# Kernel optimization log

Hardware: AMD Instinct MI355X
Metric: run time of the kernel (lower is better)

## Reference

```python
import jax, jax.numpy as jnp
import numpy as np

# Screen constants (from init_kwargs)
RES_X, RES_Y = 1024, 1024          # camera resolution (width, height)
PIX_X, PIX_Y = 1e-5, 1e-5          # pixel size in meters
BINNING = 1
NX, NY = RES_X // BINNING, RES_Y // BINNING  # effective resolution
LEFT, RIGHT = -RES_X * PIX_X / 2.0, RES_X * PIX_X / 2.0
BOTTOM, TOP = -RES_Y * PIX_Y / 2.0, RES_Y * PIX_Y / 2.0
HSTEP, VSTEP = PIX_X * BINNING, PIX_Y * BINNING
N_PARTICLES = 16_777_216
BEAM_SIGMA = 1e-3  # 1 mm rms beam size, fits in +/-5.12 mm screen extent


def setup_inputs() -> dict:
    key = jax.random.key(0)
    kx, ky = jax.random.split(key)
    xs = jax.random.normal(kx, (N_PARTICLES,), dtype=jnp.float32) * BEAM_SIGMA
    ys = jax.random.normal(ky, (N_PARTICLES,), dtype=jnp.float32) * BEAM_SIGMA
    misalignment = jnp.zeros((2,), dtype=jnp.float32)
    return {"xs": xs, "ys": ys, "misalignment": misalignment}


def reference(xs, ys, misalignment):
    # track(): subtract screen misalignment from transverse positions
    x = xs - misalignment[0]
    y = ys - misalignment[1]
    # reading(): 2D histogram over uniform pixel bin edges (torch.histogramdd)
    ix = jnp.floor((x - LEFT) / HSTEP).astype(jnp.int32)
    iy = jnp.floor((y - BOTTOM) / VSTEP).astype(jnp.int32)
    # points exactly on the rightmost/topmost edge belong to the last bin
    ix = jnp.where(x == RIGHT, NX - 1, ix)
    iy = jnp.where(y == TOP, NY - 1, iy)
    valid = (x >= LEFT) & (x <= RIGHT) & (y >= BOTTOM) & (y <= TOP)
    ix = jnp.clip(ix, 0, NX - 1)
    iy = jnp.clip(iy, 0, NY - 1)
    # image = flipud(hist.T): hist is (nx, ny) -> image[NY-1-iy, ix]
    flat = (NY - 1 - iy) * NX + ix
    w = valid.astype(jnp.float32)
    image = jnp.zeros((NY * NX,), dtype=jnp.float32).at[flat].add(w)
    return image.reshape(NY, NX)
```

## Files before the change

kernel.cpp:

```cpp
#include <hip/hip_runtime.h>
#include <hip/hip_bf16.h>


#define NXX 1024
#define NYY 1024
#define NROWS 1024
#define K3_THREADS 1024
#define K3_CHUNK 16384
#define K3_G4 (K3_CHUNK / 4)
#define K3_CAP (K3_CHUNK + 1024)
#define HCOPIES 8
#define HSTRIDE 1025

static __device__ __forceinline__ unsigned int row_of(float y) {
    const float BOTTOM = (float)(-1024.0 * 1e-5 / 2.0);
    const float TOP    = (float)( 1024.0 * 1e-5 / 2.0);
    const float INVV   = 1.0f / 1e-5f;
    if (!((y >= BOTTOM) & (y <= TOP))) return 0xFFFFFFFFu;
    int iy = __float2int_rd((y - BOTTOM) * INVV);
    iy = min(max(iy, 0), NYY - 1);
    return (unsigned int)((NYY - 1) - iy);
}

static __device__ __forceinline__ unsigned int key_of32(float x, float y) {
    unsigned int r = row_of(y);
    if (r == 0xFFFFFFFFu) return 0xFFFFFFFFu;
    const float LEFT  = (float)(-1024.0 * 1e-5 / 2.0);
    const float RIGHT = (float)( 1024.0 * 1e-5 / 2.0);
    const float INVH  = 1.0f / 1e-5f;
    unsigned int col;
    if ((x >= LEFT) & (x <= RIGHT)) {
        int ix = __float2int_rd((x - LEFT) * INVH);
        col = (unsigned int)min(max(ix, 0), NXX - 1);
    } else {
        col = 0xFFFFu;
    }
    return (r << 16) | col;
}

__global__ __launch_bounds__(256) void k1_count(
    const float4* __restrict__ ys4, const float* __restrict__ mis,
    unsigned long long* __restrict__ counts64, int n4) {
    __shared__ unsigned int lc[2 * NROWS];
    const int t = threadIdx.x;
    #pragma unroll
    for (int j = 0; j < 8; ++j) lc[t + j * 256] = 0u;
    __syncthreads();
    const unsigned int cp = (t & 1) << 10;
    const float my = mis[1];
    for (int i = blockIdx.x * blockDim.x + t; i < n4; i += gridDim.x * blockDim.x) {
        float4 yv = ys4[i];
        unsigned int r;
        r = row_of(yv.x - my); if (r != 0xFFFFFFFFu) atomicAdd(&lc[cp + r], 1u);
        r = row_of(yv.y - my); if (r != 0xFFFFFFFFu) atomicAdd(&lc[cp + r], 1u);
        r = row_of(yv.z - my); if (r != 0xFFFFFFFFu) atomicAdd(&lc[cp + r], 1u);
        r = row_of(yv.w - my); if (r != 0xFFFFFFFFu) atomicAdd(&lc[cp + r], 1u);
    }
    __syncthreads();
    #pragma unroll
    for (int p = 0; p < 2; ++p) {
        unsigned int e = lc[4 * t + 2 * p] + lc[1024 + 4 * t + 2 * p];
        unsigned int o = lc[4 * t + 2 * p + 1] + lc[1024 + 4 * t + 2 * p + 1];
        if (e | o) atomicAdd(&counts64[2 * t + p],
                             (unsigned long long)e | ((unsigned long long)o << 32));
    }
}

__global__ __launch_bounds__(1024) void k2_prefix(
    const unsigned int* __restrict__ counts,
    unsigned int* __restrict__ offsets, unsigned int* __restrict__ cursors) {
    __shared__ unsigned int waveSums[16], waveBase[16];
    const int t = threadIdx.x, lane = t & 63, wid = t >> 6;
    unsigned int c = counts[t];
    unsigned int incl = c;
    #pragma unroll
    for (int d = 1; d < 64; d <<= 1) {
        unsigned int v = __shfl_up(incl, d, 64);
        if (lane >= d) incl += v;
    }
    if (lane == 63) waveSums[wid] = incl;
    __syncthreads();
    if (t == 0) {
        unsigned int s = 0;
        #pragma unroll
        for (int i = 0; i < 16; ++i) { waveBase[i] = s; s += waveSums[i]; }
    }
    __syncthreads();
    unsigned int excl = waveBase[wid] + incl - c;
    offsets[t] = excl;
    cursors[t] = excl;
}

__global__ __launch_bounds__(K3_THREADS) void k3_scatter(
    const float4* __restrict__ xs4, const float4* __restrict__ ys4,
    const float* __restrict__ mis, unsigned int* __restrict__ cursors,
    unsigned short* __restrict__ keys, unsigned int cap) {
    __shared__ unsigned int lCount[NROWS];
    __shared__ unsigned int lAdj[NROWS];
    __shared__ unsigned int waveSums[16], waveBase[16];
    __shared__ unsigned int totalKeys;
    __shared__ unsigned int reorder[K3_CAP];

    const int t = threadIdx.x, lane = t & 63, wid = t >> 6;
    lCount[t] = 0u;
    __syncthreads();
    const float mx = mis[0], my = mis[1];

    const int base4 = blockIdx.x * K3_G4;

    float4 xv[4], yv[4];
    #pragma unroll
    for (int j = 0; j < 4; ++j) xv[j] = xs4[base4 + j * K3_THREADS + t];
    #pragma unroll
    for (int j = 0; j < 4; ++j) yv[j] = ys4[base4 + j * K3_THREADS + t];

    unsigned int mykey[16];
    #pragma unroll
    for (int j = 0; j < 4; ++j) {
        #pragma unroll
        for (int e = 0; e < 4; ++e) {
            float xx = (e == 0 ? xv[j].x : e == 1 ? xv[j].y : e == 2 ? xv[j].z : xv[j].w) - mx;
            float yy = (e == 0 ? yv[j].x : e == 1 ? yv[j].y : e == 2 ? yv[j].z : yv[j].w) - my;
            mykey[j * 4 + e] = key_of32(xx, yy);
        }
    }

    unsigned short myrank[16];
    #pragma unroll
    for (int j = 0; j < 16; ++j) {
        unsigned int k = mykey[j];
        unsigned int rk = 0;
        if (k != 0xFFFFFFFFu) rk = atomicAdd(&lCount[k >> 16], 1u);
        myrank[j] = (unsigned short)rk;
    }
    __syncthreads();

    unsigned int c0 = lCount[t];
    unsigned int p0 = (cap != 0u) ? (c0 & 1u) : 0u;
    unsigned int tt = c0 + p0;
    unsigned int b = atomicAdd(&cursors[t], tt);
    unsigned int incl = tt;
    #pragma unroll
    for (int d = 1; d < 64; d <<= 1) {
        unsigned int v = __shfl_up(incl, d, 64);
        if (lane >= d) incl += v;
    }
    if (lane == 63) waveSums[wid] = incl;
    __syncthreads();
    if (wid == 0) {
        unsigned int v = (lane < 16) ? waveSums[lane] : 0u;
        unsigned int s = v;
        #pragma unroll
        for (int d = 1; d < 16; d <<= 1) {
            unsigned int u = __shfl_up(s, d, 64);
            if (lane >= d) s += u;
        }
        if (lane < 16) waveBase[lane] = s - v;
        if (lane == 15) totalKeys = s;
    }
    __syncthreads();
    unsigned int excl = waveBase[wid] + incl - tt;
    lCount[t] = excl;
    if (cap != 0u) b += (unsigned int)t * cap;
    lAdj[t] = b - excl;
    if (p0) reorder[excl + c0] = ((unsigned int)t << 16) | 0xFFFFu;
    __syncthreads();

    #pragma unroll
    for (int j = 0; j < 16; ++j) {
        unsigned int k = mykey[j];
        if (k != 0xFFFFFFFFu) {
            reorder[lCount[k >> 16] + myrank[j]] = k;
        }
    }
    __syncthreads();

    const unsigned int total = totalKeys;
    if (cap == 0) {
        for (unsigned int j = t; j < total; j += K3_THREADS) {
            unsigned int k = reorder[j];
            keys[lAdj[k >> 16] + j] = (unsigned short)k;
        }
    } else {
        const unsigned int pairs = total >> 1;
        for (unsigned int p = t; p < pairs; p += K3_THREADS) {
            uint2 kk = *(const uint2*)&reorder[2 * p];
            unsigned int row = kk.x >> 16;
            unsigned int g = lAdj[row] + 2 * p;
            unsigned int val = (kk.x & 0xFFFFu) | (kk.y << 16);
            if (g + 2 <= (row + 1) * cap)
                *(unsigned int*)&keys[g] = val;
        }
    }
}

__global__ __launch_bounds__(1024) void k4_hist(
    const unsigned short* __restrict__ keys,
    const unsigned int* __restrict__ cnts_or_deltas,
    const unsigned int* __restrict__ offsets,
    float* __restrict__ out, unsigned int cap) {
    __shared__ unsigned int hist[HCOPIES * HSTRIDE];
    const int b = blockIdx.x;
    const int r = (b & 1) ? (512 + (b >> 1)) : (511 - (b >> 1));
    for (int t = threadIdx.x; t < HCOPIES * HSTRIDE; t += 1024) hist[t] = 0u;
    __syncthreads();
    unsigned int start, cnt;
    if (cap == 0) { start = offsets[r]; cnt = cnts_or_deltas[r]; }
    else { start = (unsigned int)r * cap; cnt = cnts_or_deltas[r];
           if (cnt > cap) cnt = cap; }
    const unsigned int copy = (threadIdx.x & (HCOPIES - 1)) * HSTRIDE;
    unsigned int head = (8u - (start & 7u)) & 7u;
    if (head > cnt) head = cnt;
    if (threadIdx.x < head) {
        unsigned int c = min((unsigned int)keys[start + threadIdx.x], 1024u);
        atomicAdd(&hist[copy + c], 1u);
    }
    const unsigned int m = cnt - head;
    const uint4* pk = (const uint4*)(keys + start + head);
    const unsigned int octs = m >> 3;
    for (unsigned int q = threadIdx.x; q < octs; q += 1024) {
        uint4 v = pk[q];
        atomicAdd(&hist[copy + min(v.x & 0xFFFFu, 1024u)], 1u);
        atomicAdd(&hist[copy + min(v.x >> 16,     1024u)], 1u);
        atomicAdd(&hist[copy + min(v.y & 0xFFFFu, 1024u)], 1u);
        atomicAdd(&hist[copy + min(v.y >> 16,     1024u)], 1u);
        atomicAdd(&hist[copy + min(v.z & 0xFFFFu, 1024u)], 1u);
        atomicAdd(&hist[copy + min(v.z >> 16,     1024u)], 1u);
        atomicAdd(&hist[copy + min(v.w & 0xFFFFu, 1024u)], 1u);
        atomicAdd(&hist[copy + min(v.w >> 16,     1024u)], 1u);
    }
    const unsigned int tail = m & 7u;
    if (threadIdx.x < tail) {
        unsigned int c = min((unsigned int)keys[start + head + (octs << 3) + threadIdx.x], 1024u);
        atomicAdd(&hist[copy + c], 1u);
    }
    __syncthreads();
    float* dst = out + (size_t)r * NXX;
    for (int v = threadIdx.x; v < NXX; v += 1024) {
        unsigned int s = 0u;
        #pragma unroll
        for (int c2 = 0; c2 < HCOPIES; ++c2) s += hist[c2 * HSTRIDE + v];
        dst[v] = (float)s;
    }
}

__global__ __launch_bounds__(256) void fallback_hist(
    const float4* __restrict__ xs4, const float4* __restrict__ ys4,
    const float* __restrict__ mis, unsigned int* __restrict__ out, int n4) {
    const float mx = mis[0], my = mis[1];
    int i = blockIdx.x * blockDim.x + threadIdx.x;
    if (i >= n4) return;
    float4 xv = xs4[i], yv = ys4[i];
    #pragma unroll
    for (int e = 0; e < 4; ++e) {
        float xx = (e == 0 ? xv.x : e == 1 ? xv.y : e == 2 ? xv.z : xv.w) - mx;
        float yy = (e == 0 ? yv.x : e == 1 ? yv.y : e == 2 ? yv.z : yv.w) - my;
        unsigned int k = key_of32(xx, yy);
        if (k != 0xFFFFFFFFu && (k & 0xFFFFu) < NXX)
            atomicAdd(&out[(k >> 16) * NXX + (k & 0xFFFFu)], 1u);
    }
}
__global__ __launch_bounds__(256) void convert_kernel(unsigned int* __restrict__ buf, int n) {
    int i = blockIdx.x * blockDim.x + threadIdx.x;
    if (i < n) { unsigned int c = buf[i]; ((float*)buf)[i] = (float)c; }
}

extern "C" void kernel_launch(void* const* d_in, const int* in_sizes, int n_in,
                              void* d_out, int out_size, void* d_ws, size_t ws_size,
                              hipStream_t stream) {
    const float* xs  = (const float*)d_in[0];
    const float* ys  = (const float*)d_in[1];
    const float* mis = (const float*)d_in[2];

    const int n  = in_sizes[0];
    const int n4 = n / 4;

    unsigned char* ws = (unsigned char*)d_ws;
    unsigned int* cursors32       = (unsigned int*)(ws);
    unsigned int* counts          = (unsigned int*)(ws);
    unsigned long long* counts64  = (unsigned long long*)(ws);
    unsigned int* offsets         = (unsigned int*)(ws + 4096);
    unsigned int* curs_ex         = (unsigned int*)(ws + 8192);
    unsigned short* keys          = (unsigned short*)(ws + 65536);

    unsigned int cap = 0;
    if (ws_size > 65536) {
        size_t c = (ws_size - 65536) / (NROWS * sizeof(unsigned short));
        c &= ~(size_t)63;
        if (c >= 73728) cap = (unsigned int)((c > 131072) ? 131072 : c);
    }

    const int k3_grid = n / K3_CHUNK;

    if (cap) {
        hipMemsetAsync(ws, 0, 4096, stream);
        k3_scatter<<<k3_grid, K3_THREADS, 0, stream>>>(
            (const float4*)xs, (const float4*)ys, mis, cursors32, keys, cap);
        k4_hist<<<NROWS, 1024, 0, stream>>>(keys, cursors32, offsets,
                                            (float*)d_out, cap);
        return;
    }

    const size_t exact_need = 65536 + (size_t)n * sizeof(unsigned short);
    if (ws_size < exact_need) {
        unsigned int* out_u = (unsigned int*)d_out;
        hipMemsetAsync(d_out, 0, (size_t)out_size * sizeof(float), stream);
        fallback_hist<<<(n4 + 255) / 256, 256, 0, stream>>>(
            (const float4*)xs, (const float4*)ys, mis, out_u, n4);
        const int npix = NXX * NYY;
        convert_kernel<<<(npix + 255) / 256, 256, 0, stream>>>(out_u, npix);
        return;
    }

    hipMemsetAsync(ws, 0, 4096, stream);
    k1_count<<<512, 256, 0, stream>>>((const float4*)ys, mis, counts64, n4);
    k2_prefix<<<1, 1024, 0, stream>>>(counts, offsets, curs_ex);
    k3_scatter<<<k3_grid, K3_THREADS, 0, stream>>>(
        (const float4*)xs, (const float4*)ys, mis, curs_ex, keys, 0u);
    k4_hist<<<NROWS, 1024, 0, stream>>>(keys, counts, offsets, (float*)d_out, 0u);
}
```

Measured before the change: 177.5 us.

## Scatter keys directly to global buckets, dropping shared-memory reorder stage

The scatter kernel no longer stages keys in a shared-memory reorder buffer with block-wide scans. Each thread now writes its 16-bit key straight to the global per-row bucket at cursor plus local rank. This removes a large LDS allocation, several barriers and the scan work, which should raise occupancy. The cost is uncoalesced, scattered 2-byte global writes instead of packed contiguous stores. The exact-count k1/k2 path is removed, so any workspace too small for the capped path now falls back to a grid-stride global atomic histogram.

```diff
diff --git a/kernel.cpp b/kernel.cpp
--- a/kernel.cpp
+++ b/kernel.cpp
@@ -1,5 +1,4 @@
 #include <hip/hip_runtime.h>
-#include <hip/hip_bf16.h>
 
 
 #define NXX 1024
@@ -8,7 +7,6 @@
 #define K3_THREADS 1024
 #define K3_CHUNK 16384
 #define K3_G4 (K3_CHUNK / 4)
-#define K3_CAP (K3_CHUNK + 1024)
 #define HCOPIES 8
 #define HSTRIDE 1025
 
@@ -38,70 +36,15 @@
     return (r << 16) | col;
 }
 
-__global__ __launch_bounds__(256) void k1_count(
-    const float4* __restrict__ ys4, const float* __restrict__ mis,
-    unsigned long long* __restrict__ counts64, int n4) {
-    __shared__ unsigned int lc[2 * NROWS];
-    const int t = threadIdx.x;
-    #pragma unroll
-    for (int j = 0; j < 8; ++j) lc[t + j * 256] = 0u;
-    __syncthreads();
-    const unsigned int cp = (t & 1) << 10;
-    const float my = mis[1];
-    for (int i = blockIdx.x * blockDim.x + t; i < n4; i += gridDim.x * blockDim.x) {
-        float4 yv = ys4[i];
-        unsigned int r;
-        r = row_of(yv.x - my); if (r != 0xFFFFFFFFu) atomicAdd(&lc[cp + r], 1u);
-        r = row_of(yv.y - my); if (r != 0xFFFFFFFFu) atomicAdd(&lc[cp + r], 1u);
-        r = row_of(yv.z - my); if (r != 0xFFFFFFFFu) atomicAdd(&lc[cp + r], 1u);
-        r = row_of(yv.w - my); if (r != 0xFFFFFFFFu) atomicAdd(&lc[cp + r], 1u);
-    }
-    __syncthreads();
-    #pragma unroll
-    for (int p = 0; p < 2; ++p) {
-        unsigned int e = lc[4 * t + 2 * p] + lc[1024 + 4 * t + 2 * p];
-        unsigned int o = lc[4 * t + 2 * p + 1] + lc[1024 + 4 * t + 2 * p + 1];
-        if (e | o) atomicAdd(&counts64[2 * t + p],
-                             (unsigned long long)e | ((unsigned long long)o << 32));
-    }
-}
-
-__global__ __launch_bounds__(1024) void k2_prefix(
-    const unsigned int* __restrict__ counts,
-    unsigned int* __restrict__ offsets, unsigned int* __restrict__ cursors) {
-    __shared__ unsigned int waveSums[16], waveBase[16];
-    const int t = threadIdx.x, lane = t & 63, wid = t >> 6;
-    unsigned int c = counts[t];
-    unsigned int incl = c;
-    #pragma unroll
-    for (int d = 1; d < 64; d <<= 1) {
-        unsigned int v = __shfl_up(incl, d, 64);
-        if (lane >= d) incl += v;
-    }
-    if (lane == 63) waveSums[wid] = incl;
-    __syncthreads();
-    if (t == 0) {
-        unsigned int s = 0;
-        #pragma unroll
-        for (int i = 0; i < 16; ++i) { waveBase[i] = s; s += waveSums[i]; }
-    }
-    __syncthreads();
-    unsigned int excl = waveBase[wid] + incl - c;
-    offsets[t] = excl;
-    cursors[t] = excl;
-}
-
 __global__ __launch_bounds__(K3_THREADS) void k3_scatter(
     const float4* __restrict__ xs4, const float4* __restrict__ ys4,
     const float* __restrict__ mis, unsigned int* __restrict__ cursors,
     unsigned short* __restrict__ keys, unsigned int cap) {
     __shared__ unsigned int lCount[NROWS];
-    __shared__ unsigned int lAdj[NROWS];
-    __shared__ unsigned int waveSums[16], waveBase[16];
-    __shared__ unsigned int totalKeys;
-    __shared__ unsigned int reorder[K3_CAP];
-
-    const int t = threadIdx.x, lane = t & 63, wid = t >> 6;
+    __shared__ unsigned int lBase[NROWS];
+    __shared__ unsigned int lLim[NROWS];
+
+    const int t = threadIdx.x;
     lCount[t] = 0u;
     __syncthreads();
     const float mx = mis[0], my = mis[1];
@@ -135,79 +78,37 @@
     }
     __syncthreads();
 
-    unsigned int c0 = lCount[t];
-    unsigned int p0 = (cap != 0u) ? (c0 & 1u) : 0u;
-    unsigned int tt = c0 + p0;
-    unsigned int b = atomicAdd(&cursors[t], tt);
-    unsigned int incl = tt;
-    #pragma unroll
-    for (int d = 1; d < 64; d <<= 1) {
-        unsigned int v = __shfl_up(incl, d, 64);
-        if (lane >= d) incl += v;
-    }
-    if (lane == 63) waveSums[wid] = incl;
-    __syncthreads();
-    if (wid == 0) {
-        unsigned int v = (lane < 16) ? waveSums[lane] : 0u;
-        unsigned int s = v;
-        #pragma unroll
-        for (int d = 1; d < 16; d <<= 1) {
-            unsigned int u = __shfl_up(s, d, 64);
-            if (lane >= d) s += u;
-        }
-        if (lane < 16) waveBase[lane] = s - v;
-        if (lane == 15) totalKeys = s;
-    }
-    __syncthreads();
-    unsigned int excl = waveBase[wid] + incl - tt;
-    lCount[t] = excl;
-    if (cap != 0u) b += (unsigned int)t * cap;
-    lAdj[t] = b - excl;
-    if (p0) reorder[excl + c0] = ((unsigned int)t << 16) | 0xFFFFu;
+    unsigned int c = lCount[t];
+    unsigned int b = 0u;
+    if (c) b = atomicAdd(&cursors[t], c);
+    lBase[t] = (unsigned int)t * cap + b;
+    lLim[t]  = (b < cap) ? (cap - b) : 0u;
     __syncthreads();
 
     #pragma unroll
     for (int j = 0; j < 16; ++j) {
         unsigned int k = mykey[j];
         if (k != 0xFFFFFFFFu) {
-            reorder[lCount[k >> 16] + myrank[j]] = k;
-        }
-    }
-    __syncthreads();
-
-    const unsigned int total = totalKeys;
-    if (cap == 0) {
-        for (unsigned int j = t; j < total; j += K3_THREADS) {
-            unsigned int k = reorder[j];
-            keys[lAdj[k >> 16] + j] = (unsigned short)k;
-        }
-    } else {
-        const unsigned int pairs = total >> 1;
-        for (unsigned int p = t; p < pairs; p += K3_THREADS) {
-            uint2 kk = *(const uint2*)&reorder[2 * p];
-            unsigned int row = kk.x >> 16;
-            unsigned int g = lAdj[row] + 2 * p;
-            unsigned int val = (kk.x & 0xFFFFu) | (kk.y << 16);
-            if (g + 2 <= (row + 1) * cap)
-                *(unsigned int*)&keys[g] = val;
+            unsigned int row = k >> 16;
+            unsigned int rk = myrank[j];
+            if (rk < lLim[row])
+                keys[lBase[row] + rk] = (unsigned short)k;
         }
     }
 }
 
 __global__ __launch_bounds__(1024) void k4_hist(
     const unsigned short* __restrict__ keys,
-    const unsigned int* __restrict__ cnts_or_deltas,
-    const unsigned int* __restrict__ offsets,
+    const unsigned int* __restrict__ cnts,
     float* __restrict__ out, unsigned int cap) {
     __shared__ unsigned int hist[HCOPIES * HSTRIDE];
     const int b = blockIdx.x;
     const int r = (b & 1) ? (512 + (b >> 1)) : (511 - (b >> 1));
     for (int t = threadIdx.x; t < HCOPIES * HSTRIDE; t += 1024) hist[t] = 0u;
     __syncthreads();
-    unsigned int start, cnt;
-    if (cap == 0) { start = offsets[r]; cnt = cnts_or_deltas[r]; }
-    else { start = (unsigned int)r * cap; cnt = cnts_or_deltas[r];
-           if (cnt > cap) cnt = cap; }
+    unsigned int start = (unsigned int)r * cap;
+    unsigned int cnt = cnts[r];
+    if (cnt > cap) cnt = cap;
     const unsigned int copy = (threadIdx.x & (HCOPIES - 1)) * HSTRIDE;
     unsigned int head = (8u - (start & 7u)) & 7u;
     if (head > cnt) head = cnt;
@@ -248,16 +149,17 @@
     const float4* __restrict__ xs4, const float4* __restrict__ ys4,
     const float* __restrict__ mis, unsigned int* __restrict__ out, int n4) {
     const float mx = mis[0], my = mis[1];
-    int i = blockIdx.x * blockDim.x + threadIdx.x;
-    if (i >= n4) return;
-    float4 xv = xs4[i], yv = ys4[i];
-    #pragma unroll
-    for (int e = 0; e < 4; ++e) {
-        float xx = (e == 0 ? xv.x : e == 1 ? xv.y : e == 2 ? xv.z : xv.w) - mx;
-        float yy = (e == 0 ? yv.x : e == 1 ? yv.y : e == 2 ? yv.z : yv.w) - my;
-        unsigned int k = key_of32(xx, yy);
-        if (k != 0xFFFFFFFFu && (k & 0xFFFFu) < NXX)
-            atomicAdd(&out[(k >> 16) * NXX + (k & 0xFFFFu)], 1u);
+    const int stride = gridDim.x * blockDim.x;
+    for (int i = blockIdx.x * blockDim.x + threadIdx.x; i < n4; i += stride) {
+        float4 xv = xs4[i], yv = ys4[i];
+        #pragma unroll
+        for (int e = 0; e < 4; ++e) {
+            float xx = (e == 0 ? xv.x : e == 1 ? xv.y : e == 2 ? xv.z : xv.w) - mx;
+            float yy = (e == 0 ? yv.x : e == 1 ? yv.y : e == 2 ? yv.z : yv.w) - my;
+            unsigned int k = key_of32(xx, yy);
+            if (k != 0xFFFFFFFFu && (k & 0xFFFFu) < NXX)
+                atomicAdd(&out[(k >> 16) * NXX + (k & 0xFFFFu)], 1u);
+        }
     }
 }
 __global__ __launch_bounds__(256) void convert_kernel(unsigned int* __restrict__ buf, int n) {
@@ -276,12 +178,8 @@
     const int n4 = n / 4;
 
     unsigned char* ws = (unsigned char*)d_ws;
-    unsigned int* cursors32       = (unsigned int*)(ws);
-    unsigned int* counts          = (unsigned int*)(ws);
-    unsigned long long* counts64  = (unsigned long long*)(ws);
-    unsigned int* offsets         = (unsigned int*)(ws + 4096);
-    unsigned int* curs_ex         = (unsigned int*)(ws + 8192);
-    unsigned short* keys          = (unsigned short*)(ws + 65536);
+    unsigned int* cursors32 = (unsigned int*)(ws);
+    unsigned short* keys    = (unsigned short*)(ws + 65536);
 
     unsigned int cap = 0;
     if (ws_size > 65536) {
@@ -296,26 +194,13 @@
         hipMemsetAsync(ws, 0, 4096, stream);
         k3_scatter<<<k3_grid, K3_THREADS, 0, stream>>>(
             (const float4*)xs, (const float4*)ys, mis, cursors32, keys, cap);
-        k4_hist<<<NROWS, 1024, 0, stream>>>(keys, cursors32, offsets,
-                                            (float*)d_out, cap);
+        k4_hist<<<NROWS, 1024, 0, stream>>>(keys, cursors32, (float*)d_out, cap);
         return;
     }
 
-    const size_t exact_need = 65536 + (size_t)n * sizeof(unsigned short);
-    if (ws_size < exact_need) {
-        unsigned int* out_u = (unsigned int*)d_out;
-        hipMemsetAsync(d_out, 0, (size_t)out_size * sizeof(float), stream);
-        fallback_hist<<<(n4 + 255) / 256, 256, 0, stream>>>(
-            (const float4*)xs, (const float4*)ys, mis, out_u, n4);
-        const int npix = NXX * NYY;
-        convert_kernel<<<(npix + 255) / 256, 256, 0, stream>>>(out_u, npix);
-        return;
-    }
-
-    hipMemsetAsync(ws, 0, 4096, stream);
-    k1_count<<<512, 256, 0, stream>>>((const float4*)ys, mis, counts64, n4);
-    k2_prefix<<<1, 1024, 0, stream>>>(counts, offsets, curs_ex);
-    k3_scatter<<<k3_grid, K3_THREADS, 0, stream>>>(
-        (const float4*)xs, (const float4*)ys, mis, curs_ex, keys, 0u);
-    k4_hist<<<NROWS, 1024, 0, stream>>>(keys, counts, offsets, (float*)d_out, 0u);
-}
+    unsigned int* out_u = (unsigned int*)d_out;
+    hipMemsetAsync(d_out, 0, (size_t)NXX * NYY * sizeof(float), stream);
+    fallback_hist<<<2048, 256, 0, stream>>>(
+        (const float4*)xs, (const float4*)ys, mis, out_u, n4);
+    convert_kernel<<<(NXX * NYY + 255) / 256, 256, 0, stream>>>(out_u, NXX * NYY);
+}
```

After: 225.3 us. 1.27x slower.
